# Kernel optimization log

Measured on AMD Instinct MI355X. Metric: run time of the kernel, lower is better.

The kernel has to match this reference:

```python
import jax, jax.numpy as jnp
import numpy as np

K = 3
STRIDE = 1
PAD = 1


def _bilinear_gather(x, ys, xs):
    # x: [B,C,H,W]; ys, xs: [B,n,Ho,Wo] float sample positions. Zero padding outside.
    B, C, H, W = x.shape
    y0 = jnp.floor(ys)
    x0 = jnp.floor(xs)
    wy1 = ys - y0
    wx1 = xs - x0
    x_flat = x.reshape(B, C, H * W)

    def corner(yc, xc, w):
        valid = (yc >= 0) & (yc <= H - 1) & (xc >= 0) & (xc <= W - 1)
        yi = jnp.clip(yc, 0, H - 1).astype(jnp.int32)
        xi = jnp.clip(xc, 0, W - 1).astype(jnp.int32)
        idx = (yi * W + xi).reshape(B, 1, -1)
        vals = jnp.take_along_axis(x_flat, jnp.broadcast_to(idx, (B, C, idx.shape[-1])), axis=2)
        vals = vals.reshape(B, C, *ys.shape[1:])  # [B,C,n,Ho,Wo]
        return vals * (w * valid)[:, None]

    return (corner(y0, x0, (1 - wy1) * (1 - wx1))
            + corner(y0, x0 + 1, (1 - wy1) * wx1)
            + corner(y0 + 1, x0, wy1 * (1 - wx1))
            + corner(y0 + 1, x0 + 1, wy1 * wx1))


def setup_inputs() -> dict:
    key = jax.random.key(0)
    k1, k2, k3, k4 = jax.random.split(key, 4)
    B, Cin, Cout, H, W = 16, 128, 128, 64, 64
    n = K * K
    x = jax.random.normal(k1, (B, Cin, H, W), dtype=jnp.float32)
    # main deform-conv weight (kaiming-ish scale) and bias
    fan_in = Cin * n
    weight = jax.random.normal(k2, (Cout, Cin, K, K), dtype=jnp.float32) * np.float32(np.sqrt(2.0 / fan_in))
    bias = jnp.zeros((Cout,), dtype=jnp.float32)
    # offset/mask predicting conv (small init so offsets are modest)
    off_w = jax.random.normal(k3, (3 * n, Cin, K, K), dtype=jnp.float32) * np.float32(0.01)
    off_b = jax.random.normal(k4, (3 * n,), dtype=jnp.float32) * np.float32(0.01)
    return {"x": x, "weight": weight, "bias": bias, "off_w": off_w, "off_b": off_b}


def reference(x, weight, bias, off_w, off_b):
    B, Cin, H, W = x.shape
    Cout = weight.shape[0]
    n = K * K
    Ho = (H + 2 * PAD - K) // STRIDE + 1
    Wo = (W + 2 * PAD - K) // STRIDE + 1

    # offset / mask prediction conv
    out = jax.lax.conv_general_dilated(
        x, off_w, window_strides=(STRIDE, STRIDE), padding=((PAD, PAD), (PAD, PAD)),
        dimension_numbers=("NCHW", "OIHW", "NCHW"))
    out = out + off_b[None, :, None, None]  # [B, 3n, Ho, Wo]
    offset = out[:, :2 * n].reshape(B, n, 2, Ho, Wo)  # per-tap (dy, dx)
    mask = jax.nn.sigmoid(out[:, 2 * n:])  # [B, n, Ho, Wo]

    # base sampling grid per kernel tap
    t = jnp.arange(n)
    py = (t // K).astype(jnp.float32)[:, None] + (jnp.arange(Ho) * STRIDE - PAD).astype(jnp.float32)[None, :]  # [n,Ho]
    px = (t % K).astype(jnp.float32)[:, None] + (jnp.arange(Wo) * STRIDE - PAD).astype(jnp.float32)[None, :]   # [n,Wo]
    ys = py[None, :, :, None] + offset[:, :, 0]  # [B,n,Ho,Wo]
    xs = px[None, :, None, :] + offset[:, :, 1]

    sampled = _bilinear_gather(x, ys, xs)            # [B,C,n,Ho,Wo]
    sampled = sampled * mask[:, None]                # modulated (DCNv2)
    w = weight.reshape(Cout, Cin, n)
    y = jnp.einsum("bcnhw,ocn->bohw", sampled, w)
    return y + bias[None, :, None, None]
```

## Files before the change

kernel.cpp:

```cpp
#include <hip/hip_runtime.h>
#include <hip/hip_fp16.h>


typedef unsigned int u32;
typedef __attribute__((ext_vector_type(8))) _Float16 f16x8;
typedef __attribute__((ext_vector_type(4))) float f32x4;

union U16 { uint4 u; f16x8 h; };
union H2U { __half2 h2; u32 u; };

static __device__ __forceinline__ u32 pkh(float a, float b) {
    H2U c; c.h2 = __float22half2_rn(make_float2(a, b)); return c.u;
}
static __device__ __forceinline__ u32 h1(float f) {
    return (u32)__half_as_ushort(__float2half_rn(f));
}
static __device__ __forceinline__ u32 hfma2u(u32 a, u32 w, u32 acc) {
    H2U x, y, z; x.u = a; y.u = w; z.u = acc;
    z.h2 = __hfma2(x.h2, y.h2, z.h2); return z.u;
}
static __device__ __forceinline__ u32 hmul2u(u32 a, u32 w) {
    H2U x, y; x.u = a; y.u = w;
    y.h2 = __hmul2(x.h2, y.h2); return y.u;
}

#define B_   16
#define HW_  4096
#define CU_  64

__global__ __launch_bounds__(256) void k_transpose(const float* __restrict__ x,
                                                   u32* __restrict__ xtu) {
    __shared__ float tile[32][129];
    int blk = blockIdx.x, t = threadIdx.x;
    int b = blk >> 7, hw0 = (blk & 127) << 5;
    int hwl = t & 31, cg = t >> 5;
    const float* src = x + (size_t)b * 128 * HW_ + hw0 + hwl;
#pragma unroll
    for (int i = 0; i < 16; ++i) { int c = cg + (i << 3); tile[hwl][c] = src[(size_t)c * HW_]; }
    __syncthreads();
    u32* dst = xtu + ((size_t)b * HW_ + hw0) * CU_;
    int u = t & 63, hq = t >> 6;
#pragma unroll
    for (int j = 0; j < 8; ++j) {
        int hw = (hq << 3) + j;
        dst[(size_t)hw * CU_ + u] = pkh(tile[hw][2 * u], tile[hw][2 * u + 1]);
    }
}

__global__ __launch_bounds__(256) void k_prep(const float* __restrict__ weight,
                                              const float* __restrict__ off_w,
                                              uint4* __restrict__ wtv,
                                              u32* __restrict__ woffu) {
    int idx = blockIdx.x * 256 + threadIdx.x;
    if (idx < 18432) {
        int l = idx & 63, og = (idx >> 6) & 7, ks = (idx >> 9) & 3, n = idx >> 11;
        int o = og * 16 + (l & 15);
        int c0 = ks * 32 + (l >> 4) * 8;
        u32 r[4];
#pragma unroll
        for (int q = 0; q < 4; ++q) {
            int c = c0 + 2 * q;
            r[q] = pkh(weight[((size_t)(o * 128 + c)) * 9 + n],
                       weight[((size_t)(o * 128 + c + 1)) * 9 + n]);
        }
        wtv[idx] = make_uint4(r[0], r[1], r[2], r[3]);
    } else {
        int k = idx - 18432;
        int o = k / 576, r = k % 576;
        int tap = r / 64, cu = r % 64, c = cu * 2;
        u32 v = 0u;
        if (o < 27) {
            float a = off_w[((size_t)(o * 128 + c)) * 9 + tap];
            float b = off_w[((size_t)(o * 128 + c + 1)) * 9 + tap];
            v = pkh(a, b);
        }
        woffu[k] = v;
    }
}

__global__ __launch_bounds__(256) void k_offconv(const u32* __restrict__ xtu,
                                                 const u32* __restrict__ woffu,
                                                 const float* __restrict__ off_b,
                                                 float* __restrict__ offout) {
    __shared__ __align__(16) u32 S[3][64][64];
    int blk = ((blockIdx.x & 7) << 7) + (blockIdx.x >> 3);
    int t = threadIdx.x;
    int b = blk >> 6, ho = blk & 63;
    const u32* xb = xtu + (size_t)b * HW_ * CU_;
    const uint4 z4 = {0u, 0u, 0u, 0u};
#pragma unroll
    for (int i = 0; i < 12; ++i) {
        int li = t + (i << 8);
        int r = li >> 10, rem = li & 1023;
        int px = rem >> 4, ch = rem & 15;
        int yy = ho + r - 1;
        uint4 v = ((unsigned)yy < 64u) ? *(const uint4*)(xb + ((yy << 6) + px) * CU_ + (ch << 2)) : z4;
        *(uint4*)&S[r][px][(ch ^ (px & 7)) << 2] = v;
    }
    __syncthreads();
    int lane = t & 63, w = t >> 6, l15 = lane & 15, lhi = lane >> 4;
    int ob = w >> 1, pb0 = (w & 1) << 1;
    f32x4 acc[2];
    acc[0] = (f32x4){0.f, 0.f, 0.f, 0.f};
    acc[1] = (f32x4){0.f, 0.f, 0.f, 0.f};
#pragma unroll 1
    for (int tap = 0; tap < 9; ++tap) {
        int ky = tap / 3, kx = tap % 3;
        int yy = ho + ky - 1;
        if ((unsigned)yy >= 64u) continue;
        U16 af[4];
#pragma unroll
        for (int ks = 0; ks < 4; ++ks)
            af[ks].u = *(const uint4*)(woffu + (size_t)(ob * 16 + l15) * 576
                                       + tap * 64 + ks * 16 + lhi * 4);
#pragma unroll
        for (int pp = 0; pp < 2; ++pp) {
            int pr = ((pb0 + pp) << 4) + l15;
            int pxs = pr + kx - 1;
            bool v = (unsigned)pxs < 64u;
            int pxc = v ? pxs : 0;
#pragma unroll
            for (int ks = 0; ks < 4; ++ks) {
                U16 sf;
                sf.u = v ? *(const uint4*)&S[ky][pxc][((ks * 4 + lhi) ^ (pxc & 7)) << 2] : z4;
                acc[pp] = __builtin_amdgcn_mfma_f32_16x16x32_f16(af[ks].h, sf.h, acc[pp], 0, 0, 0);
            }
        }
    }
    float* dst = offout + (size_t)b * 27 * HW_ + (ho << 6);
#pragma unroll
    for (int pp = 0; pp < 2; ++pp)
#pragma unroll
        for (int r = 0; r < 4; ++r) {
            int o = ob * 16 + lhi * 4 + r;
            if (o < 27) {
                float s = acc[pp][r] + off_b[o];
                if (o >= 18) s = 1.f / (1.f + __expf(-s));
                dst[(size_t)o * HW_ + ((pb0 + pp) << 4) + l15] = s;
            }
        }
}

__global__ __launch_bounds__(256) void k_params(const float* __restrict__ offout,
                                                uint4* __restrict__ paramsP) {
    int g = blockIdx.x * 256 + threadIdx.x;
    int wo = g & 63, r = g >> 6;
    int tap = r % 9, bho = r / 9;
    int ho = bho & 63, b = bho >> 6;
    const float* ob_ = offout + (size_t)b * 27 * HW_ + ho * 64 + wo;
    float dy = ob_[(size_t)(2 * tap) * HW_];
    float dx = ob_[(size_t)(2 * tap + 1) * HW_];
    float m  = ob_[(size_t)(18 + tap) * HW_];
    float ys = (float)(ho + tap / 3 - 1) + dy;
    float xs = (float)(wo + tap % 3 - 1) + dx;
    float y0f = floorf(ys), x0f = floorf(xs);
    float fy = ys - y0f, fx = xs - x0f;
    int y0 = (int)y0f, x0 = (int)x0f;
    bool vy0 = (unsigned)y0 < 64u, vy1 = (unsigned)(y0 + 1) < 64u;
    bool vx0 = (unsigned)x0 < 64u, vx1 = (unsigned)(x0 + 1) < 64u;
    u32 h00 = h1((vy0 && vx0) ? (1.f - fy) * (1.f - fx) * m : 0.f);
    u32 h01 = h1((vy0 && vx1) ? (1.f - fy) * fx * m : 0.f);
    u32 h10 = h1((vy1 && vx0) ? fy * (1.f - fx) * m : 0.f);
    u32 h11 = h1((vy1 && vx1) ? fy * fx * m : 0.f);
    int y0c = min(max(y0, 0), 63), y1c = min(max(y0 + 1, 0), 63);
    int x0c = min(max(x0, 0), 63), x1c = min(max(x0 + 1, 0), 63);
    u32 a0 = ((u32)y0c << 6) | (u32)x0c;
    u32 a1 = ((u32)y1c << 6) | (u32)x1c;
    u32 idx4 = ((((u32)(b << 6) + ho) * 9 + tap) * 256 + ((wo >> 3) << 5) + ((wo & 7) << 2)) >> 2;
    paramsP[idx4] = make_uint4(h00 | (h01 << 16), h10 | (h11 << 16), a0 | (a1 << 12), 0u);
}

__global__ __launch_bounds__(512, 4) void k_fused(const u32* __restrict__ xtu,
                                                  const uint4* __restrict__ wtv,
                                                  const u32* __restrict__ paramsP,
                                                  const float* __restrict__ bias,
                                                  float* __restrict__ out) {
    __shared__ __align__(16) u32 S[2][64][68];
    __shared__ __align__(16) u32 PRM[8][2][32];
    int blk = ((blockIdx.x & 7) << 7) + (blockIdx.x >> 3);
    int t = threadIdx.x;
    int b = blk >> 6, ho = blk & 63;
    int w = t >> 6, lane = t & 63, l15 = lane & 15, lhi = lane >> 4;
    int o0 = w << 4;
    int lane4 = lane << 2;
    int l31 = lane & 31;

    f32x4 acc[4];
#pragma unroll
    for (int pb = 0; pb < 4; ++pb) acc[pb] = (f32x4){0.f, 0.f, 0.f, 0.f};

    const char* xbb = (const char*)(xtu + (size_t)b * HW_ * CU_);
    const u32* pP = paramsP + (size_t)(((b << 6) + ho) * 9) * 256 + (w << 5) + l31;

    u32 ld[8][4];

#define ISSUE_G(NB)                                                          \
    _Pragma("unroll") for (int j = 0; j < 8; ++j) {                          \
        u32 w2 = PRM[w][NB][(j << 2) + 2];                                   \
        u32 a0 = (w2 & 0xFFFu) << 8;                                         \
        u32 a1 = ((w2 >> 12) & 0xFFFu) << 8;                                 \
        u32 a01 = (a0 & ~0x3FFFu) | (a1 & 0x3FFFu);                          \
        u32 a10 = (a1 & ~0x3FFFu) | (a0 & 0x3FFFu);                          \
        ld[j][0] = *(const u32*)(xbb + a0 + lane4);                          \
        ld[j][1] = *(const u32*)(xbb + a01 + lane4);                         \
        ld[j][2] = *(const u32*)(xbb + a10 + lane4);                         \
        ld[j][3] = *(const u32*)(xbb + a1 + lane4);                          \
    }

    PRM[w][0][l31] = pP[0];
    __builtin_amdgcn_sched_barrier(0);
    ISSUE_G(0);
    u32 prNext = pP[256];

#pragma unroll 1
    for (int n = 0; n < 9; ++n) {
        int buf = n & 1;
        U16 wf[4];
#pragma unroll
        for (int ks = 0; ks < 4; ++ks)
            wf[ks].u = wtv[(((n << 2) + ks) * 8 + w) * 64 + lane];
        __builtin_amdgcn_sched_barrier(0);
#pragma unroll
        for (int j = 0; j < 8; ++j) {
            uint4 P = *(const uint4*)&PRM[w][buf][j << 2];
            u32 w00p = (P.x & 0xFFFFu) | (P.x << 16);
            u32 w01p = (P.x >> 16) | (P.x & 0xFFFF0000u);
            u32 w10p = (P.y & 0xFFFFu) | (P.y << 16);
            u32 w11p = (P.y >> 16) | (P.y & 0xFFFF0000u);
            u32 r = hfma2u(ld[j][3], w11p, hfma2u(ld[j][2], w10p,
                    hfma2u(ld[j][1], w01p, hmul2u(ld[j][0], w00p))));
            S[buf][(w << 3) + j][lane] = r;
        }
        if (n < 8) PRM[w][buf ^ 1][l31] = prNext;
        if (n < 7) prNext = pP[(size_t)(n + 2) * 256];
        if (n < 8) { ISSUE_G(buf ^ 1); }
        asm volatile("s_waitcnt lgkmcnt(0)" ::: "memory");
        __builtin_amdgcn_sched_barrier(0);
        __builtin_amdgcn_s_barrier();
        __builtin_amdgcn_sched_barrier(0);
#pragma unroll
        for (int ks = 0; ks < 4; ++ks) {
            U16 sf[4];
#pragma unroll
            for (int pb = 0; pb < 4; ++pb)
                sf[pb].u = *(const uint4*)&S[buf][pb * 16 + l15][(ks * 4 + lhi) << 2];
#pragma unroll
            for (int pb = 0; pb < 4; ++pb)
                acc[pb] = __builtin_amdgcn_mfma_f32_16x16x32_f16(
                    wf[ks].h, sf[pb].h, acc[pb], 0, 0, 0);
        }
    }
#undef ISSUE_G
    float* ob_base = out + (size_t)b * 128 * HW_ + ho * 64;
#pragma unroll
    for (int r = 0; r < 4; ++r) {
        int o = o0 + lhi * 4 + r;
        float bv = bias[o];
#pragma unroll
        for (int pb = 0; pb < 4; ++pb)
            ob_base[(size_t)o * HW_ + pb * 16 + l15] = acc[pb][r] + bv;
    }
}

extern "C" void kernel_launch(void* const* d_in, const int* in_sizes, int n_in,
                              void* d_out, int out_size, void* d_ws, size_t ws_size,
                              hipStream_t stream) {
    const float* x      = (const float*)d_in[0];
    const float* weight = (const float*)d_in[1];
    const float* bias   = (const float*)d_in[2];
    const float* off_w  = (const float*)d_in[3];
    const float* off_b  = (const float*)d_in[4];
    float* out = (float*)d_out;

    u32*   xtu     = (u32*)d_ws;
    float* offout  = (float*)(xtu + (size_t)B_ * HW_ * CU_);
    uint4* wtv     = (uint4*)(offout + (size_t)B_ * 27 * HW_);
    u32*   woffu   = (u32*)wtv + 73728;
    uint4* paramsP = (uint4*)(woffu + 18432);

    hipLaunchKernelGGL(k_transpose, dim3(2048), dim3(256), 0, stream, x, xtu);
    hipLaunchKernelGGL(k_prep, dim3(144), dim3(256), 0, stream, weight, off_w, wtv, woffu);
    hipLaunchKernelGGL(k_offconv, dim3(1024), dim3(256), 0, stream, xtu, woffu, off_b, offout);
    hipLaunchKernelGGL(k_params, dim3(2304), dim3(256), 0, stream, offout, paramsP);
    hipLaunchKernelGGL(k_fused, dim3(1024), dim3(512), 0, stream, xtu, wtv,
                       (const u32*)paramsP, bias, out);
}
```

Before: 107.6 us.

## Fuse bilinear parameter computation into offset conv and pre-broadcast half2 weights

The offset conv now writes its 27-channel output into shared memory and computes the bilinear weights and corner addresses in place, which removes the separate k_params kernel, its launch, and the float round trip through global memory. Corner weights are stored pre-duplicated as half2, so the fused kernel loads them directly instead of unpacking them with shifts and masks. This doubles the per-tap parameter record (512 words instead of 256) and the PRM shared buffer, and adds shared memory and a barrier to the offset conv.

```diff
diff --git a/kernel.cpp b/kernel.cpp
--- a/kernel.cpp
+++ b/kernel.cpp
@@ -12,8 +12,9 @@
 static __device__ __forceinline__ u32 pkh(float a, float b) {
     H2U c; c.h2 = __float22half2_rn(make_float2(a, b)); return c.u;
 }
-static __device__ __forceinline__ u32 h1(float f) {
-    return (u32)__half_as_ushort(__float2half_rn(f));
+static __device__ __forceinline__ u32 pkw(float w) {
+    __half h = __float2half_rn(w);
+    H2U c; c.h2 = __half2(h, h); return c.u;
 }
 static __device__ __forceinline__ u32 hfma2u(u32 a, u32 w, u32 acc) {
     H2U x, y, z; x.u = a; y.u = w; z.u = acc;
@@ -81,8 +82,9 @@
 __global__ __launch_bounds__(256) void k_offconv(const u32* __restrict__ xtu,
                                                  const u32* __restrict__ woffu,
                                                  const float* __restrict__ off_b,
-                                                 float* __restrict__ offout) {
+                                                 u32* __restrict__ params) {
     __shared__ __align__(16) u32 S[3][64][64];
+    __shared__ float OFF[27][65];
     int blk = ((blockIdx.x & 7) << 7) + (blockIdx.x >> 3);
     int t = threadIdx.x;
     int b = blk >> 6, ho = blk & 63;
@@ -127,7 +129,6 @@
             }
         }
     }
-    float* dst = offout + (size_t)b * 27 * HW_ + (ho << 6);
 #pragma unroll
     for (int pp = 0; pp < 2; ++pp)
 #pragma unroll
@@ -136,69 +137,69 @@
             if (o < 27) {
                 float s = acc[pp][r] + off_b[o];
                 if (o >= 18) s = 1.f / (1.f + __expf(-s));
-                dst[(size_t)o * HW_ + ((pb0 + pp) << 4) + l15] = s;
+                OFF[o][((pb0 + pp) << 4) + l15] = s;
             }
         }
-}
-
-__global__ __launch_bounds__(256) void k_params(const float* __restrict__ offout,
-                                                uint4* __restrict__ paramsP) {
-    int g = blockIdx.x * 256 + threadIdx.x;
-    int wo = g & 63, r = g >> 6;
-    int tap = r % 9, bho = r / 9;
-    int ho = bho & 63, b = bho >> 6;
-    const float* ob_ = offout + (size_t)b * 27 * HW_ + ho * 64 + wo;
-    float dy = ob_[(size_t)(2 * tap) * HW_];
-    float dx = ob_[(size_t)(2 * tap + 1) * HW_];
-    float m  = ob_[(size_t)(18 + tap) * HW_];
-    float ys = (float)(ho + tap / 3 - 1) + dy;
-    float xs = (float)(wo + tap % 3 - 1) + dx;
-    float y0f = floorf(ys), x0f = floorf(xs);
-    float fy = ys - y0f, fx = xs - x0f;
-    int y0 = (int)y0f, x0 = (int)x0f;
-    bool vy0 = (unsigned)y0 < 64u, vy1 = (unsigned)(y0 + 1) < 64u;
-    bool vx0 = (unsigned)x0 < 64u, vx1 = (unsigned)(x0 + 1) < 64u;
-    u32 h00 = h1((vy0 && vx0) ? (1.f - fy) * (1.f - fx) * m : 0.f);
-    u32 h01 = h1((vy0 && vx1) ? (1.f - fy) * fx * m : 0.f);
-    u32 h10 = h1((vy1 && vx0) ? fy * (1.f - fx) * m : 0.f);
-    u32 h11 = h1((vy1 && vx1) ? fy * fx * m : 0.f);
-    int y0c = min(max(y0, 0), 63), y1c = min(max(y0 + 1, 0), 63);
-    int x0c = min(max(x0, 0), 63), x1c = min(max(x0 + 1, 0), 63);
-    u32 a0 = ((u32)y0c << 6) | (u32)x0c;
-    u32 a1 = ((u32)y1c << 6) | (u32)x1c;
-    u32 idx4 = ((((u32)(b << 6) + ho) * 9 + tap) * 256 + ((wo >> 3) << 5) + ((wo & 7) << 2)) >> 2;
-    paramsP[idx4] = make_uint4(h00 | (h01 << 16), h10 | (h11 << 16), a0 | (a1 << 12), 0u);
+    __syncthreads();
+    u32* pbase = params + ((size_t)((b << 6) + ho) * 9) * 512;
+#pragma unroll 1
+    for (int it = 0; it < 3; ++it) {
+        int item = it * 256 + t;
+        if (item < 576) {
+            int tap = item >> 6, px = item & 63;
+            float dy = OFF[2 * tap][px];
+            float dx = OFF[2 * tap + 1][px];
+            float m  = OFF[18 + tap][px];
+            float ys = (float)(ho + tap / 3 - 1) + dy;
+            float xs = (float)(px + tap % 3 - 1) + dx;
+            float y0f = floorf(ys), x0f = floorf(xs);
+            float fy = ys - y0f, fx = xs - x0f;
+            int y0 = (int)y0f, x0 = (int)x0f;
+            bool vy0 = (unsigned)y0 < 64u, vy1 = (unsigned)(y0 + 1) < 64u;
+            bool vx0 = (unsigned)x0 < 64u, vx1 = (unsigned)(x0 + 1) < 64u;
+            u32 w00p = pkw((vy0 && vx0) ? (1.f - fy) * (1.f - fx) * m : 0.f);
+            u32 w01p = pkw((vy0 && vx1) ? (1.f - fy) * fx * m : 0.f);
+            u32 w10p = pkw((vy1 && vx0) ? fy * (1.f - fx) * m : 0.f);
+            u32 w11p = pkw((vy1 && vx1) ? fy * fx * m : 0.f);
+            int y0c = min(max(y0, 0), 63), y1c = min(max(y0 + 1, 0), 63);
+            int x0c = min(max(x0, 0), 63), x1c = min(max(x0 + 1, 0), 63);
+            u32 a0 = ((u32)y0c << 6) | (u32)x0c;
+            u32 a1 = ((u32)y1c << 6) | (u32)x1c;
+            u32* dst = pbase + (size_t)tap * 512 + ((px >> 3) << 6);
+            *(uint4*)&dst[(px & 7) << 2] = make_uint4(w00p, w01p, w10p, w11p);
+            dst[32 + (px & 7)] = a0 | (a1 << 12);
+        }
+    }
 }
 
 __global__ __launch_bounds__(512, 4) void k_fused(const u32* __restrict__ xtu,
                                                   const uint4* __restrict__ wtv,
-                                                  const u32* __restrict__ paramsP,
+                                                  const u32* __restrict__ params,
                                                   const float* __restrict__ bias,
                                                   float* __restrict__ out) {
     __shared__ __align__(16) u32 S[2][64][68];
-    __shared__ __align__(16) u32 PRM[8][2][32];
+    __shared__ __align__(16) u32 PRM[8][2][64];
     int blk = ((blockIdx.x & 7) << 7) + (blockIdx.x >> 3);
     int t = threadIdx.x;
     int b = blk >> 6, ho = blk & 63;
     int w = t >> 6, lane = t & 63, l15 = lane & 15, lhi = lane >> 4;
     int o0 = w << 4;
     int lane4 = lane << 2;
-    int l31 = lane & 31;
 
     f32x4 acc[4];
 #pragma unroll
     for (int pb = 0; pb < 4; ++pb) acc[pb] = (f32x4){0.f, 0.f, 0.f, 0.f};
 
     const char* xbb = (const char*)(xtu + (size_t)b * HW_ * CU_);
-    const u32* pP = paramsP + (size_t)(((b << 6) + ho) * 9) * 256 + (w << 5) + l31;
+    const u32* pP = params + (size_t)(((b << 6) + ho) * 9) * 512 + (w << 6) + lane;
 
     u32 ld[8][4];
 
 #define ISSUE_G(NB)                                                          \
     _Pragma("unroll") for (int j = 0; j < 8; ++j) {                          \
-        u32 w2 = PRM[w][NB][(j << 2) + 2];                                   \
-        u32 a0 = (w2 & 0xFFFu) << 8;                                         \
-        u32 a1 = ((w2 >> 12) & 0xFFFu) << 8;                                 \
+        u32 A = PRM[w][NB][32 + j];                                          \
+        u32 a0 = (A & 0xFFFu) << 8;                                          \
+        u32 a1 = ((A >> 12) & 0xFFFu) << 8;                                  \
         u32 a01 = (a0 & ~0x3FFFu) | (a1 & 0x3FFFu);                          \
         u32 a10 = (a1 & ~0x3FFFu) | (a0 & 0x3FFFu);                          \
         ld[j][0] = *(const u32*)(xbb + a0 + lane4);                          \
@@ -207,10 +208,10 @@
         ld[j][3] = *(const u32*)(xbb + a1 + lane4);                          \
     }
 
-    PRM[w][0][l31] = pP[0];
+    PRM[w][0][lane] = pP[0];
     __builtin_amdgcn_sched_barrier(0);
     ISSUE_G(0);
-    u32 prNext = pP[256];
+    u32 prNext = pP[512];
 
 #pragma unroll 1
     for (int n = 0; n < 9; ++n) {
@@ -222,17 +223,13 @@
         __builtin_amdgcn_sched_barrier(0);
 #pragma unroll
         for (int j = 0; j < 8; ++j) {
-            uint4 P = *(const uint4*)&PRM[w][buf][j << 2];
-            u32 w00p = (P.x & 0xFFFFu) | (P.x << 16);
-            u32 w01p = (P.x >> 16) | (P.x & 0xFFFF0000u);
-            u32 w10p = (P.y & 0xFFFFu) | (P.y << 16);
-            u32 w11p = (P.y >> 16) | (P.y & 0xFFFF0000u);
-            u32 r = hfma2u(ld[j][3], w11p, hfma2u(ld[j][2], w10p,
-                    hfma2u(ld[j][1], w01p, hmul2u(ld[j][0], w00p))));
+            uint4 ww = *(const uint4*)&PRM[w][buf][j << 2];
+            u32 r = hfma2u(ld[j][3], ww.w, hfma2u(ld[j][2], ww.z,
+                    hfma2u(ld[j][1], ww.y, hmul2u(ld[j][0], ww.x))));
             S[buf][(w << 3) + j][lane] = r;
         }
-        if (n < 8) PRM[w][buf ^ 1][l31] = prNext;
-        if (n < 7) prNext = pP[(size_t)(n + 2) * 256];
+        if (n < 8) PRM[w][buf ^ 1][lane] = prNext;
+        if (n < 7) prNext = pP[(size_t)(n + 2) * 512];
         if (n < 8) { ISSUE_G(buf ^ 1); }
         asm volatile("s_waitcnt lgkmcnt(0)" ::: "memory");
         __builtin_amdgcn_sched_barrier(0);
@@ -272,16 +269,13 @@
     const float* off_b  = (const float*)d_in[4];
     float* out = (float*)d_out;
 
-    u32*   xtu     = (u32*)d_ws;
-    float* offout  = (float*)(xtu + (size_t)B_ * HW_ * CU_);
-    uint4* wtv     = (uint4*)(offout + (size_t)B_ * 27 * HW_);
-    u32*   woffu   = (u32*)wtv + 73728;
-    uint4* paramsP = (uint4*)(woffu + 18432);
+    u32*   xtu    = (u32*)d_ws;
+    uint4* wtv    = (uint4*)(xtu + (size_t)B_ * HW_ * CU_);
+    u32*   woffu  = (u32*)wtv + 73728;
+    u32*   params = woffu + 18432;
 
     hipLaunchKernelGGL(k_transpose, dim3(2048), dim3(256), 0, stream, x, xtu);
     hipLaunchKernelGGL(k_prep, dim3(144), dim3(256), 0, stream, weight, off_w, wtv, woffu);
-    hipLaunchKernelGGL(k_offconv, dim3(1024), dim3(256), 0, stream, xtu, woffu, off_b, offout);
-    hipLaunchKernelGGL(k_params, dim3(2304), dim3(256), 0, stream, offout, paramsP);
-    hipLaunchKernelGGL(k_fused, dim3(1024), dim3(512), 0, stream, xtu, wtv,
-                       (const u32*)paramsP, bias, out);
-}
+    hipLaunchKernelGGL(k_offconv, dim3(1024), dim3(256), 0, stream, xtu, woffu, off_b, params);
+    hipLaunchKernelGGL(k_fused, dim3(1024), dim3(512), 0, stream, xtu, wtv, params, bias, out);
+}
```

New measurement: 92.30 us. 14.2% less time.
